# Performance work log

Measured on AMD Instinct MI355X. Metric: run time of the kernel, lower is better.

The kernel has to match this reference:

```python
import jax, jax.numpy as jnp
import numpy as np

H = 16  # n_head

def _rms_norm(x):
    eps = jnp.asarray(jnp.finfo(x.dtype).eps, x.dtype)
    ms = jnp.mean(jnp.square(x), axis=-1, keepdims=True)
    return x * jax.lax.rsqrt(ms + eps)

def _interp(x, pos):
    # x: [B,T,H,Dh]; pos: [B,T,H,Dh] float positions along axis 1
    T = x.shape[1]
    pos_floor = jnp.floor(pos)
    pos0 = jnp.clip(pos_floor, 0, T - 1).astype(jnp.int32)
    pos1 = jnp.clip(pos0 + 1, 0, T - 1)
    frac = pos - pos_floor
    x0 = jnp.take_along_axis(x, pos0, axis=1)
    x1 = jnp.take_along_axis(x, pos1, axis=1)
    return x0 + (x1 - x0) * frac

def setup_inputs() -> dict:
    key = jax.random.key(0)
    ks = jax.random.split(key, 5)
    B, T, D = 4, 4096, 2048
    x = jax.random.normal(ks[0], (B, T, D), dtype=jnp.float32)
    scale = 0.02
    Wq = jax.random.normal(ks[1], (D, D), dtype=jnp.float32) * scale
    Wk = jax.random.normal(ks[2], (D, D), dtype=jnp.float32) * scale
    Wsq = jax.random.normal(ks[3], (D, D), dtype=jnp.float32) * scale
    Wsk = jax.random.normal(ks[4], (D, D), dtype=jnp.float32) * scale
    return {"x": x, "Wq": Wq, "Wk": Wk, "Wsq": Wsq, "Wsk": Wsk}

def reference(x, Wq, Wk, Wsq, Wsk):
    B, T, D = x.shape
    Dh = D // H
    # projections (Linear with weight [out,in]: y = x @ W.T)
    q = _rms_norm((x @ Wq.T).reshape(B, T, H, Dh))
    k = _rms_norm((x @ Wk.T).reshape(B, T, H, Dh))
    sq = jax.nn.softplus(x @ Wsq.T).reshape(B, T, H, Dh)
    sk = jax.nn.softplus(x @ Wsk.T).reshape(B, T, H, Dh)
    t_idx = jnp.arange(T, dtype=x.dtype).reshape(1, T, 1, 1)
    posq = jnp.minimum(jnp.maximum(t_idx - sq, 0.0), t_idx)
    posk = jnp.minimum(jnp.maximum(t_idx - sk, 0.0), t_idx)
    q_def = _interp(q, posq)
    k_def = _interp(k, posk)
    return (q_def * k_def).reshape(B, T, D)
```

## Files before the change

kernel.cpp:

```cpp
#include <hip/hip_runtime.h>

typedef unsigned short u16;
typedef __bf16 bf16x8 __attribute__((ext_vector_type(8)));
typedef unsigned short u16x8 __attribute__((ext_vector_type(8)));
typedef unsigned short u16x4 __attribute__((ext_vector_type(4)));
typedef float f32x4 __attribute__((ext_vector_type(4)));

#define K_DIM 2048
#define BM 128
#define BN 128
#define BK 32

#define GLL16(g, l) __builtin_amdgcn_global_load_lds( \
    (const __attribute__((address_space(1))) void*)(g), \
    (__attribute__((address_space(3))) void*)(l), 16, 0, 0)

__device__ __forceinline__ u16 f2bf(float f) {
    unsigned int u = __builtin_bit_cast(unsigned int, f);
    u = (u + 0x7fffu + ((u >> 16) & 1u)) >> 16;
    return (u16)u;
}
__device__ __forceinline__ float bf2f(u16 h) {
    unsigned int u = ((unsigned int)h) << 16;
    return __builtin_bit_cast(float, u);
}
__device__ __forceinline__ float softplus_f(float v) {
    return fmaxf(v, 0.0f) + log1pf(expf(-fabsf(v)));
}

__global__ void pack_kernel(const float* __restrict__ src, u16* __restrict__ dst, int n4) {
    int i = blockIdx.x * blockDim.x + threadIdx.x;
    if (i >= n4) return;
    float4 v = ((const float4*)src)[i];
    u16x4 o;
    o[0] = f2bf(v.x); o[1] = f2bf(v.y); o[2] = f2bf(v.z); o[3] = f2bf(v.w);
    ((u16x4*)dst)[i] = o;
}

__global__ __launch_bounds__(256) void gemm_fused(
    const u16* __restrict__ xb, const u16* __restrict__ wb,
    u16* __restrict__ qb, u16* __restrict__ kb,
    u16* __restrict__ sqb, u16* __restrict__ skb)
{
    __shared__ u16 Als[BM * BK];
    __shared__ u16 Bls[BM * BK];
    __shared__ float ss[BM];

    const int tid  = threadIdx.x;
    const int lane = tid & 63;
    const int wave = tid >> 6;
    const int wm = wave >> 1;
    const int wn = wave & 1;
    const int gm0 = blockIdx.y * BM;
    const int gn0 = blockIdx.x * BN;

    const int r0 = tid >> 2;
    const int qs = ((tid & 3) - ((tid >> 3) & 3)) & 3;
    const int kc = qs * 8;
    const u16* gA0 = xb + (size_t)(gm0 + r0) * K_DIM + kc;
    const u16* gA1 = gA0 + (size_t)64 * K_DIM;
    const u16* gB0 = wb + (size_t)(gn0 + r0) * K_DIM + kc;
    const u16* gB1 = gB0 + (size_t)64 * K_DIM;
    char* lA0 = (char*)Als + wave * 1024;
    char* lA1 = (char*)Als + 4096 + wave * 1024;
    char* lB0 = (char*)Bls + wave * 1024;
    char* lB1 = (char*)Bls + 4096 + wave * 1024;

    f32x4 acc[4][4] = {};

    const int mr = lane & 15;
    const int q  = lane >> 4;
    const int s  = (q + (mr >> 1)) & 3;
    const int fragoff = mr * 32 + s * 8;

    for (int kt = 0; kt < K_DIM / BK; ++kt) {
        GLL16(gA0, lA0); GLL16(gA1, lA1);
        GLL16(gB0, lB0); GLL16(gB1, lB1);
        gA0 += BK; gA1 += BK; gB0 += BK; gB1 += BK;
        __syncthreads();

        bf16x8 a[4], b[4];
#pragma unroll
        for (int i = 0; i < 4; ++i)
            a[i] = __builtin_bit_cast(bf16x8, *(const u16x8*)&Als[(wm * 4 + i) * 512 + fragoff]);
#pragma unroll
        for (int j = 0; j < 4; ++j)
            b[j] = __builtin_bit_cast(bf16x8, *(const u16x8*)&Bls[(wn * 4 + j) * 512 + fragoff]);
#pragma unroll
        for (int i = 0; i < 4; ++i)
#pragma unroll
            for (int j = 0; j < 4; ++j)
                acc[i][j] = __builtin_amdgcn_mfma_f32_16x16x32_bf16(a[i], b[j], acc[i][j], 0, 0, 0);
        __syncthreads();
    }

    const int which = gn0 >> 11;
    if (tid < BM) ss[tid] = 0.0f;
    __syncthreads();

    const int mbase = wm * 64 + (lane >> 4) * 4;
    const int col0  = (gn0 & 2047) + wn * 64 + (lane & 15);

    if (which < 2) {
#pragma unroll
        for (int i = 0; i < 4; ++i) {
#pragma unroll
            for (int r = 0; r < 4; ++r) {
                float sv = acc[i][0][r] * acc[i][0][r] + acc[i][1][r] * acc[i][1][r]
                         + acc[i][2][r] * acc[i][2][r] + acc[i][3][r] * acc[i][3][r];
                sv += __shfl_xor(sv, 1, 64);
                sv += __shfl_xor(sv, 2, 64);
                sv += __shfl_xor(sv, 4, 64);
                sv += __shfl_xor(sv, 8, 64);
                if ((lane & 15) == 0) atomicAdd(&ss[mbase + i * 16 + r], sv);
            }
        }
        __syncthreads();
    }

    u16* ob = (which == 0) ? qb : (which == 1) ? kb : (which == 2) ? sqb : skb;
#pragma unroll
    for (int i = 0; i < 4; ++i) {
#pragma unroll
        for (int r = 0; r < 4; ++r) {
            int m = mbase + i * 16 + r;
            size_t rowbase = (size_t)(gm0 + m) * 2048;
            float scale = 1.0f;
            if (which < 2)
                scale = rsqrtf(ss[m] * (1.0f / 128.0f) + 1.1920929e-07f);
#pragma unroll
            for (int j = 0; j < 4; ++j) {
                float v = acc[i][j][r];
                v = (which < 2) ? v * scale : softplus_f(v);
                ob[rowbase + col0 + j * 16] = f2bf(v);
            }
        }
    }
}

__global__ void interp_mul(const u16* __restrict__ qb, const u16* __restrict__ kb,
                           const u16* __restrict__ sqb, const u16* __restrict__ skb,
                           float* __restrict__ out)
{
    size_t idx = (size_t)blockIdx.x * 256 + threadIdx.x;
    int c = (int)(idx & 2047);
    size_t bt = idx >> 11;
    int t = (int)(bt & 4095);
    float tf = (float)t;

    float sqv = bf2f(sqb[idx]);
    float skv = bf2f(skb[idx]);
    float pq = fminf(fmaxf(tf - sqv, 0.0f), tf);
    float pk = fminf(fmaxf(tf - skv, 0.0f), tf);
    float pqf = floorf(pq), pkf = floorf(pk);
    int q0i = (int)pqf, k0i = (int)pkf;
    int q1i = min(q0i + 1, 4095), k1i = min(k0i + 1, 4095);
    float fq = pq - pqf, fk = pk - pkf;

    size_t rb = (idx >> 23) << 23;
    size_t o = rb + (size_t)c;
    float q0 = bf2f(qb[o + ((size_t)q0i << 11)]);
    float q1 = bf2f(qb[o + ((size_t)q1i << 11)]);
    float k0 = bf2f(kb[o + ((size_t)k0i << 11)]);
    float k1 = bf2f(kb[o + ((size_t)k1i << 11)]);
    float qd = q0 + (q1 - q0) * fq;
    float kd = k0 + (k1 - k0) * fk;
    out[idx] = qd * kd;
}

extern "C" void kernel_launch(void* const* d_in, const int* in_sizes, int n_in,
                              void* d_out, int out_size, void* d_ws, size_t ws_size,
                              hipStream_t stream) {
    const float* x   = (const float*)d_in[0];
    const float* Wq  = (const float*)d_in[1];
    const float* Wk  = (const float*)d_in[2];
    const float* Wsq = (const float*)d_in[3];
    const float* Wsk = (const float*)d_in[4];
    float* out = (float*)d_out;

    const size_t NEED = 369098752;
    if (ws_size < NEED) return;
    char* ws = (char*)d_ws;
    u16* xb  = (u16*)(ws);
    u16* wb  = (u16*)(ws + 67108864);
    u16* qb  = (u16*)(ws + 100663296);
    u16* kb  = (u16*)(ws + 167772160);
    u16* sqb = (u16*)(ws + 234881024);
    u16* skb = (u16*)(ws + 301989888);

    pack_kernel<<<32768, 256, 0, stream>>>(x,   xb, 8388608);
    pack_kernel<<<4096,  256, 0, stream>>>(Wq,  wb,            1048576);
    pack_kernel<<<4096,  256, 0, stream>>>(Wk,  wb + 4194304,  1048576);
    pack_kernel<<<4096,  256, 0, stream>>>(Wsq, wb + 8388608,  1048576);
    pack_kernel<<<4096,  256, 0, stream>>>(Wsk, wb + 12582912, 1048576);

    dim3 ggrid(64, 128);
    gemm_fused<<<ggrid, 256, 0, stream>>>(xb, wb, qb, kb, sqb, skb);

    interp_mul<<<131072, 256, 0, stream>>>(qb, kb, sqb, skb, out);
}
```

Baseline: 1.172 ms.

## Double GEMM K-tile, merge pack launches, vectorize interp kernel

Raises the GEMM K-tile from 32 to 64 with a new 8-way swizzled LDS layout, so each loop iteration issues twice the MFMA work per pair of barriers and the barrier count is halved. The five pack launches are merged into one kernel to cut launch overhead. The interpolation kernel now handles 8 elements per thread, using vector loads for sq/sk and float4 stores. Doubling LDS use per block may lower occupancy, and the new swizzle has to stay bank-conflict free.

After: 1.295 ms. 10.5% more time.

```diff
diff --git a/kernel.cpp b/kernel.cpp
--- a/kernel.cpp
+++ b/kernel.cpp
@@ -9,7 +9,7 @@
 #define K_DIM 2048
 #define BM 128
 #define BN 128
-#define BK 32
+#define BK 64
 
 #define GLL16(g, l) __builtin_amdgcn_global_load_lds( \
     (const __attribute__((address_space(1))) void*)(g), \
@@ -28,9 +28,22 @@
     return fmaxf(v, 0.0f) + log1pf(expf(-fabsf(v)));
 }
 
-__global__ void pack_kernel(const float* __restrict__ src, u16* __restrict__ dst, int n4) {
-    int i = blockIdx.x * blockDim.x + threadIdx.x;
-    if (i >= n4) return;
+__global__ void pack_all(const float* __restrict__ x,
+                         const float* __restrict__ Wq, const float* __restrict__ Wk,
+                         const float* __restrict__ Wsq, const float* __restrict__ Wsk,
+                         u16* __restrict__ xb, u16* __restrict__ wb) {
+    int b = blockIdx.x;
+    const float* src; u16* dst; size_t i;
+    if (b < 32768) {
+        src = x; dst = xb;
+        i = (size_t)b * 256 + threadIdx.x;
+    } else {
+        int w  = (b - 32768) >> 12;
+        int bb = (b - 32768) & 4095;
+        src = (w < 2) ? ((w == 0) ? Wq : Wk) : ((w == 2) ? Wsq : Wsk);
+        dst = wb + (size_t)w * 4194304;
+        i = (size_t)bb * 256 + threadIdx.x;
+    }
     float4 v = ((const float4*)src)[i];
     u16x4 o;
     o[0] = f2bf(v.x); o[1] = f2bf(v.y); o[2] = f2bf(v.z); o[3] = f2bf(v.w);
@@ -54,38 +67,55 @@
     const int gm0 = blockIdx.y * BM;
     const int gn0 = blockIdx.x * BN;
 
-    const int r0 = tid >> 2;
-    const int qs = ((tid & 3) - ((tid >> 3) & 3)) & 3;
+    const int r0 = tid >> 3;
+    const int qs = ((tid & 7) - ((tid >> 3) & 7)) & 7;
     const int kc = qs * 8;
-    const u16* gA0 = xb + (size_t)(gm0 + r0) * K_DIM + kc;
-    const u16* gA1 = gA0 + (size_t)64 * K_DIM;
-    const u16* gB0 = wb + (size_t)(gn0 + r0) * K_DIM + kc;
-    const u16* gB1 = gB0 + (size_t)64 * K_DIM;
-    char* lA0 = (char*)Als + wave * 1024;
-    char* lA1 = (char*)Als + 4096 + wave * 1024;
-    char* lB0 = (char*)Bls + wave * 1024;
-    char* lB1 = (char*)Bls + 4096 + wave * 1024;
+    const u16* gA = xb + (size_t)(gm0 + r0) * K_DIM + kc;
+    const u16* gB = wb + (size_t)(gn0 + r0) * K_DIM + kc;
+    const size_t rstep = (size_t)32 * K_DIM;
+    char* lA = (char*)Als + wave * 1024;
+    char* lB = (char*)Bls + wave * 1024;
 
     f32x4 acc[4][4] = {};
 
     const int mr = lane & 15;
     const int q  = lane >> 4;
-    const int s  = (q + (mr >> 1)) & 3;
-    const int fragoff = mr * 32 + s * 8;
+    const int m7 = mr & 7;
+    const int pos0 = ((q + m7) & 7) * 8;
+    const int pos1 = ((q + m7 + 4) & 7) * 8;
+    const int abase = (wm * 64 + mr) * 64;
+    const int bbase = (wn * 64 + mr) * 64;
 
     for (int kt = 0; kt < K_DIM / BK; ++kt) {
-        GLL16(gA0, lA0); GLL16(gA1, lA1);
-        GLL16(gB0, lB0); GLL16(gB1, lB1);
-        gA0 += BK; gA1 += BK; gB0 += BK; gB1 += BK;
+        GLL16(gA,             lA);
+        GLL16(gA + rstep,     lA + 4096);
+        GLL16(gA + 2 * rstep, lA + 8192);
+        GLL16(gA + 3 * rstep, lA + 12288);
+        GLL16(gB,             lB);
+        GLL16(gB + rstep,     lB + 4096);
+        GLL16(gB + 2 * rstep, lB + 8192);
+        GLL16(gB + 3 * rstep, lB + 12288);
+        gA += BK; gB += BK;
         __syncthreads();
 
         bf16x8 a[4], b[4];
 #pragma unroll
         for (int i = 0; i < 4; ++i)
-            a[i] = __builtin_bit_cast(bf16x8, *(const u16x8*)&Als[(wm * 4 + i) * 512 + fragoff]);
+            a[i] = __builtin_bit_cast(bf16x8, *(const u16x8*)&Als[abase + i * 1024 + pos0]);
 #pragma unroll
         for (int j = 0; j < 4; ++j)
-            b[j] = __builtin_bit_cast(bf16x8, *(const u16x8*)&Bls[(wn * 4 + j) * 512 + fragoff]);
+            b[j] = __builtin_bit_cast(bf16x8, *(const u16x8*)&Bls[bbase + j * 1024 + pos0]);
+#pragma unroll
+        for (int i = 0; i < 4; ++i)
+#pragma unroll
+            for (int j = 0; j < 4; ++j)
+                acc[i][j] = __builtin_amdgcn_mfma_f32_16x16x32_bf16(a[i], b[j], acc[i][j], 0, 0, 0);
+#pragma unroll
+        for (int i = 0; i < 4; ++i)
+            a[i] = __builtin_bit_cast(bf16x8, *(const u16x8*)&Als[abase + i * 1024 + pos1]);
+#pragma unroll
+        for (int j = 0; j < 4; ++j)
+            b[j] = __builtin_bit_cast(bf16x8, *(const u16x8*)&Bls[bbase + j * 1024 + pos1]);
 #pragma unroll
         for (int i = 0; i < 4; ++i)
 #pragma unroll
@@ -142,30 +172,35 @@
                            const u16* __restrict__ sqb, const u16* __restrict__ skb,
                            float* __restrict__ out)
 {
-    size_t idx = (size_t)blockIdx.x * 256 + threadIdx.x;
-    int c = (int)(idx & 2047);
-    size_t bt = idx >> 11;
+    size_t base = ((size_t)blockIdx.x * 256 + threadIdx.x) * 8;
+    int c0 = (int)(base & 2047);
+    size_t bt = base >> 11;
     int t = (int)(bt & 4095);
     float tf = (float)t;
 
-    float sqv = bf2f(sqb[idx]);
-    float skv = bf2f(skb[idx]);
-    float pq = fminf(fmaxf(tf - sqv, 0.0f), tf);
-    float pk = fminf(fmaxf(tf - skv, 0.0f), tf);
-    float pqf = floorf(pq), pkf = floorf(pk);
-    int q0i = (int)pqf, k0i = (int)pkf;
-    int q1i = min(q0i + 1, 4095), k1i = min(k0i + 1, 4095);
-    float fq = pq - pqf, fk = pk - pkf;
-
-    size_t rb = (idx >> 23) << 23;
-    size_t o = rb + (size_t)c;
-    float q0 = bf2f(qb[o + ((size_t)q0i << 11)]);
-    float q1 = bf2f(qb[o + ((size_t)q1i << 11)]);
-    float k0 = bf2f(kb[o + ((size_t)k0i << 11)]);
-    float k1 = bf2f(kb[o + ((size_t)k1i << 11)]);
-    float qd = q0 + (q1 - q0) * fq;
-    float kd = k0 + (k1 - k0) * fk;
-    out[idx] = qd * kd;
+    u16x8 sq8 = *(const u16x8*)(sqb + base);
+    u16x8 sk8 = *(const u16x8*)(skb + base);
+    size_t rb = (base >> 23) << 23;
+
+    float res[8];
+#pragma unroll
+    for (int e = 0; e < 8; ++e) {
+        float pq = fminf(fmaxf(tf - bf2f(sq8[e]), 0.0f), tf);
+        float pk = fminf(fmaxf(tf - bf2f(sk8[e]), 0.0f), tf);
+        float pqf = floorf(pq), pkf = floorf(pk);
+        int q0i = (int)pqf, k0i = (int)pkf;
+        int q1i = min(q0i + 1, 4095), k1i = min(k0i + 1, 4095);
+        float fq = pq - pqf, fk = pk - pkf;
+        size_t o = rb + (size_t)(c0 + e);
+        float q0 = bf2f(qb[o + ((size_t)q0i << 11)]);
+        float q1 = bf2f(qb[o + ((size_t)q1i << 11)]);
+        float k0 = bf2f(kb[o + ((size_t)k0i << 11)]);
+        float k1 = bf2f(kb[o + ((size_t)k1i << 11)]);
+        res[e] = (q0 + (q1 - q0) * fq) * (k0 + (k1 - k0) * fk);
+    }
+    float4* op = (float4*)(out + base);
+    op[0] = make_float4(res[0], res[1], res[2], res[3]);
+    op[1] = make_float4(res[4], res[5], res[6], res[7]);
 }
 
 extern "C" void kernel_launch(void* const* d_in, const int* in_sizes, int n_in,
@@ -188,14 +223,10 @@
     u16* sqb = (u16*)(ws + 234881024);
     u16* skb = (u16*)(ws + 301989888);
 
-    pack_kernel<<<32768, 256, 0, stream>>>(x,   xb, 8388608);
-    pack_kernel<<<4096,  256, 0, stream>>>(Wq,  wb,            1048576);
-    pack_kernel<<<4096,  256, 0, stream>>>(Wk,  wb + 4194304,  1048576);
-    pack_kernel<<<4096,  256, 0, stream>>>(Wsq, wb + 8388608,  1048576);
-    pack_kernel<<<4096,  256, 0, stream>>>(Wsk, wb + 12582912, 1048576);
+    pack_all<<<49152, 256, 0, stream>>>(x, Wq, Wk, Wsq, Wsk, xb, wb);
 
     dim3 ggrid(64, 128);
     gemm_fused<<<ggrid, 256, 0, stream>>>(xb, wb, qb, kb, sqb, skb);
 
-    interp_mul<<<131072, 256, 0, stream>>>(qb, kb, sqb, skb, out);
-}
+    interp_mul<<<16384, 256, 0, stream>>>(qb, kb, sqb, skb, out);
+}
```
